# Kernel tuning notes

Measured on AMD Instinct MI355X. Metric: run time of the kernel, lower is better.

Reference implementation:

```python
import jax, jax.numpy as jnp
import numpy as np
from jax import lax

D_MODEL = 768
BATCH = 16
SEQ = 2048
N_BLOCKS = D_MODEL // 3
LN_EPS = 1e-5


def setup_inputs() -> dict:
    key = jax.random.key(0)
    ks = jax.random.split(key, 4)
    scale = 1.0 / np.sqrt(D_MODEL)
    x = jax.random.normal(ks[0], (BATCH, SEQ, D_MODEL), dtype=jnp.float32)
    W_biv = jax.random.normal(ks[1], (D_MODEL, D_MODEL), dtype=jnp.float32) * scale
    b_biv = jnp.zeros((D_MODEL,), dtype=jnp.float32)
    W_decay = jax.random.normal(ks[2], (1, D_MODEL), dtype=jnp.float32) * scale
    b_decay = jnp.full((1,), 1.4, dtype=jnp.float32)  # nn.init.constant_(decay_proj.bias, 1.4)
    W_in = jax.random.normal(ks[3], (D_MODEL, D_MODEL), dtype=jnp.float32) * scale
    b_in = jnp.zeros((D_MODEL,), dtype=jnp.float32)
    ln_gamma = jnp.ones((D_MODEL,), dtype=jnp.float32)
    ln_beta = jnp.zeros((D_MODEL,), dtype=jnp.float32)
    return {"x": x, "W_biv": W_biv, "b_biv": b_biv, "W_decay": W_decay,
            "b_decay": b_decay, "W_in": W_in, "b_in": b_in,
            "ln_gamma": ln_gamma, "ln_beta": ln_beta}


def _quat_rotate_blocks(h_blocks, biv):
    """h_blocks, biv: (batch, n_blocks, 3) -> rotated (batch, n_blocks, 3)."""
    norm_b = jnp.maximum(jnp.linalg.norm(biv, axis=-1, keepdims=True), 1e-8)
    half = norm_b * 0.5
    w = jnp.cos(half)[..., 0]
    s = (jnp.sin(half) / norm_b)[..., 0]
    # note the original maps bivector components in reversed order
    qx = s * biv[..., 2]
    qy = -s * biv[..., 1]
    qz = s * biv[..., 0]
    vx, vy, vz = h_blocks[..., 0], h_blocks[..., 1], h_blocks[..., 2]
    tx = 2.0 * (qy * vz - qz * vy)
    ty = 2.0 * (qz * vx - qx * vz)
    tz = 2.0 * (qx * vy - qy * vx)
    rx = vx + w * tx + (qy * tz - qz * ty)
    ry = vy + w * ty + (qz * tx - qx * tz)
    rz = vz + w * tz + (qx * ty - qy * tx)
    return jnp.stack([rx, ry, rz], axis=-1)


def reference(x, W_biv, b_biv, W_decay, b_decay, W_in, b_in, ln_gamma, ln_beta):
    B, S, D = x.shape
    nb = D // 3
    # precompute all per-timestep projections as big GEMMs
    biv = (jnp.einsum('bsd,ed->bse', x, W_biv) + b_biv).reshape(B, S, nb, 3)
    decay = jax.nn.sigmoid(jnp.einsum('bsd,ed->bse', x, W_decay) + b_decay)  # (B,S,1)
    inj = jnp.einsum('bsd,ed->bse', x, W_in) + b_in  # (B,S,D)

    def step(h, t):
        biv_t, decay_t, inj_t = t
        rot = _quat_rotate_blocks(h.reshape(B, nb, 3), biv_t).reshape(B, D)
        h_next = decay_t * rot + inj_t
        return h_next, h_next

    xs = (jnp.moveaxis(biv, 1, 0), jnp.moveaxis(decay, 1, 0), jnp.moveaxis(inj, 1, 0))
    h0 = jnp.zeros((B, D), dtype=x.dtype)
    _, out = lax.scan(step, h0, xs)  # (S,B,D)
    out = jnp.moveaxis(out, 0, 1)  # (B,S,D)

    mean = jnp.mean(out, axis=-1, keepdims=True)
    var = jnp.mean(jnp.square(out - mean), axis=-1, keepdims=True)
    normed = (out - mean) * lax.rsqrt(var + LN_EPS) * ln_gamma + ln_beta
    return normed + x
```

## Files before the change

kernel.cpp:

```cpp
#include <hip/hip_runtime.h>
#include <stdint.h>

#define D_MODEL 768
#define BATCH   16
#define SEQ     2048
#define M_ROWS  (BATCH * SEQ)
#define LN_EPS  1e-5f

#define CHUNKS  64
#define CLEN    (SEQ / CHUNKS)
#define PFB     8

typedef __attribute__((ext_vector_type(4))) float        f32x4;
typedef __attribute__((ext_vector_type(8))) __bf16       bf16x8;
typedef __attribute__((ext_vector_type(2))) unsigned int u32x2;

__device__ __forceinline__ unsigned short f2bf(float f) {
    union { float f; uint32_t u; } v; v.f = f;
    uint32_t u = v.u;
    uint32_t r = (u + 0x7FFFu + ((u >> 16) & 1u)) >> 16;
    return (unsigned short)r;
}
__device__ __forceinline__ float bf2f(unsigned short u) {
    union { uint32_t u; float f; } v; v.u = (uint32_t)u << 16; return v.f;
}
__device__ __forceinline__ float bfx(u32x2 v, int k) {
    unsigned int w = (k & 2) ? v[1] : v[0];
    return bf2f((unsigned short)(w >> ((k & 1) * 16)));
}

__device__ __forceinline__ void gload_lds16(const void* g, void* l) {
    __builtin_amdgcn_global_load_lds(
        (const __attribute__((address_space(1))) unsigned int*)g,
        (__attribute__((address_space(3))) unsigned int*)l,
        16, 0, 0);
}

__global__ __launch_bounds__(256) void k_conv_decay(
    const float* __restrict__ x, const float* __restrict__ Wd,
    const float* __restrict__ bd, unsigned short* __restrict__ xb,
    float* __restrict__ decay)
{
    int row = blockIdx.x;
    int i   = threadIdx.x;
    const float* xr = x + (size_t)row * D_MODEL;
    float v0 = xr[i], v1 = xr[i + 256], v2 = xr[i + 512];
    unsigned short* xbr = xb + (size_t)row * D_MODEL;
    xbr[i] = f2bf(v0); xbr[i + 256] = f2bf(v1); xbr[i + 512] = f2bf(v2);

    float part = v0 * Wd[i] + v1 * Wd[i + 256] + v2 * Wd[i + 512];
    #pragma unroll
    for (int off = 32; off; off >>= 1) part += __shfl_down(part, off);
    __shared__ float wsum[4];
    int wid = i >> 6, lane = i & 63;
    if (lane == 0) wsum[wid] = part;
    __syncthreads();
    if (i == 0) {
        float s = wsum[0] + wsum[1] + wsum[2] + wsum[3] + bd[0];
        decay[row] = 1.f / (1.f + __expf(-s));
    }
}

__global__ __launch_bounds__(256) void k_conv_w(
    const float* __restrict__ Wb, const float* __restrict__ Wi,
    unsigned short* __restrict__ Wdst)
{
    const int NW = D_MODEL * D_MODEL;
    int g = blockIdx.x * 256 + threadIdx.x;
    int base = g * 4;
    unsigned short* dst = Wdst + base;
    const float* src;
    if (base < NW) { src = Wb + base; }
    else           { src = Wi + (base - NW); }
    float4 v = *(const float4*)src;
    ushort4 o;
    o.x = f2bf(v.x); o.y = f2bf(v.y); o.z = f2bf(v.z); o.w = f2bf(v.w);
    *(ushort4*)dst = o;
}

#define GBM 256
#define GBN 256
#define GNBX 6
#define GNBY 128
#define NT   12

__global__ __launch_bounds__(512, 2) void k_gemm_fused(
    const unsigned short* __restrict__ A,
    const unsigned short* __restrict__ Bw,
    const float* __restrict__ bias_biv, const float* __restrict__ bias_in,
    u32x2* __restrict__ bivq, u32x2* __restrict__ injq)
{
    extern __shared__ unsigned short LDSBUF[];
    unsigned short* LA = LDSBUF;
    unsigned short* LB = LDSBUF + 32768;

    int id  = blockIdx.x;
    int swz = (id & 7) * 96 + (id >> 3);
    int bxc = swz % GNBX, byr = swz / GNBX;
    int m0 = byr * GBM, n0 = bxc * GBN;

    int tid  = threadIdx.x;
    int wid  = tid >> 6, lane = tid & 63;
    int wm = wid >> 2, wn = wid & 3;
    int rl = lane & 15, kq = lane >> 4;
    int sl = kq ^ ((rl >> 1) & 3);
    int aoff = (wm * 128 + rl) * 32 + sl * 8;
    int boff = (wn * 64  + rl) * 32 + sl * 8;

    f32x4 acc[8][4] = {};

    #define STAGE_HALF(DBUF, KT, HH) do {                                        \
        _Pragma("unroll")                                                        \
        for (int p = 0; p < 2; ++p) {                                            \
            int idx = p * 512 + tid;                                             \
            int row = idx >> 2;                                                  \
            int ss  = ((idx & 3) ^ ((idx >> 3) & 3)) * 8;  \
            gload_lds16(A  + (size_t)(m0 + row) * D_MODEL + (KT) * 64 + (HH) * 32 + ss, \
                        LA + (DBUF) * 16384 + (HH) * 8192 + idx * 8);            \
            gload_lds16(Bw + (size_t)(n0 + row) * D_MODEL + (KT) * 64 + (HH) * 32 + ss, \
                        LB + (DBUF) * 16384 + (HH) * 8192 + idx * 8);            \
        }                                                                        \
    } while (0)

    #define PHASE(D, H, DOSTAGE, SBUF, SKT, SHH, WAITSTR) do {                   \
        bf16x8 af[8], bfv[4];                                                    \
        const unsigned short* pa = LA + (D) * 16384 + (H) * 8192 + aoff;         \
        const unsigned short* pb = LB + (D) * 16384 + (H) * 8192 + boff;         \
        _Pragma("unroll")                                                        \
        for (int i = 0; i < 8; ++i) af[i]  = *(const bf16x8*)(pa + i * 512);     \
        _Pragma("unroll")                                                        \
        for (int j = 0; j < 4; ++j) bfv[j] = *(const bf16x8*)(pb + j * 512);     \
        if (DOSTAGE) STAGE_HALF(SBUF, SKT, SHH);                                 \
        asm volatile(WAITSTR ::: "memory");                                      \
        asm volatile("s_barrier" ::: "memory");                                  \
        asm volatile("s_waitcnt lgkmcnt(0)" ::: "memory");                       \
        __builtin_amdgcn_sched_barrier(0);                                       \
        __builtin_amdgcn_s_setprio(1);                                           \
        _Pragma("unroll")                                                        \
        for (int i = 0; i < 8; ++i)                                              \
            _Pragma("unroll")                                                    \
            for (int j = 0; j < 4; ++j)                                          \
                acc[i][j] = __builtin_amdgcn_mfma_f32_16x16x32_bf16(             \
                    af[i], bfv[j], acc[i][j], 0, 0, 0);                          \
        __builtin_amdgcn_s_setprio(0);                                           \
        asm volatile("s_barrier" ::: "memory");                                  \
    } while (0)

    STAGE_HALF(0, 0, 0);
    STAGE_HALF(0, 0, 1);
    STAGE_HALF(1, 1, 0);
    asm volatile("s_waitcnt vmcnt(8)" ::: "memory");
    asm volatile("s_barrier" ::: "memory");

    for (int t = 0; t < 10; ++t) {
        int cur = t & 1;
        PHASE(cur, 0, true, cur ^ 1, t + 1, 1, "s_waitcnt vmcnt(8)");
        PHASE(cur, 1, true, cur,     t + 2, 0, "s_waitcnt vmcnt(8)");
    }
    PHASE(0, 0, true,  1, 11, 1, "s_waitcnt vmcnt(8)");
    PHASE(0, 1, false, 0, 0,  0, "s_waitcnt vmcnt(4)");
    PHASE(1, 0, false, 0, 0,  0, "s_waitcnt vmcnt(0)");
    PHASE(1, 1, false, 0, 0,  0, "");

    #undef PHASE
    #undef STAGE_HALF

    u32x2* Cq; const float* bias; int nloc;
    if (n0 < D_MODEL) { Cq = bivq; bias = bias_biv; nloc = n0; }
    else              { Cq = injq; bias = bias_in;  nloc = n0 - D_MODEL; }
    int cl = lane & 15;
    int qbase = (m0 >> 2) + wm * 32 + (lane >> 4);
    #pragma unroll
    for (int j = 0; j < 4; ++j) {
        int col = nloc + wn * 64 + j * 16 + cl;
        float bs = bias[col];
        #pragma unroll
        for (int i = 0; i < 8; ++i) {
            f32x4 a = acc[i][j];
            unsigned int lo = (unsigned int)f2bf(a[0] + bs) | ((unsigned int)f2bf(a[1] + bs) << 16);
            unsigned int hi = (unsigned int)f2bf(a[2] + bs) | ((unsigned int)f2bf(a[3] + bs) << 16);
            u32x2 pk = {lo, hi};
            Cq[(size_t)(qbase + i * 4) * D_MODEL + col] = pk;
        }
    }
}

#define QSTEP_CORE(BX,BY,BZ, IX,IY,IZ, DD)                              \
    {   float n2   = (BX)*(BX) + (BY)*(BY) + (BZ)*(BZ);                 \
        float nrm  = fmaxf(__builtin_sqrtf(n2), 1e-8f);                 \
        float half = 0.5f * nrm;                                        \
        float w = __cosf(half);                                         \
        float s = __sinf(half) / nrm;                                   \
        float qx = s * (BZ), qy = -s * (BY), qz = s * (BX);             \
        float tx = 2.f * (qy * hz - qz * hy);                           \
        float ty = 2.f * (qz * hx - qx * hz);                           \
        float tz = 2.f * (qx * hy - qy * hx);                           \
        float rx = hx + w * tx + (qy * tz - qz * ty);                   \
        float ry = hy + w * ty + (qz * tx - qx * tz);                   \
        float rz = hz + w * tz + (qx * ty - qy * tx);                   \
        hx = fmaf((DD), rx, (IX));                                      \
        hy = fmaf((DD), ry, (IY));                                      \
        hz = fmaf((DD), rz, (IZ));                                      \
        float nQw = w * Qw - qx * Qx - qy * Qy - qz * Qz;               \
        float nQx = w * Qx + Qw * qx + (qy * Qz - qz * Qy);             \
        float nQy = w * Qy + Qw * qy + (qz * Qx - qx * Qz);             \
        float nQz = w * Qz + Qw * qz + (qx * Qy - qy * Qx);             \
        Qw = nQw; Qx = nQx; Qy = nQy; Qz = nQz;                         \
        S *= (DD);                                                      \
    }

#define QSTEP_H(BX,BY,BZ, IX,IY,IZ, DD)                                 \
    {   float n2   = (BX)*(BX) + (BY)*(BY) + (BZ)*(BZ);                 \
        float nrm  = fmaxf(__builtin_sqrtf(n2), 1e-8f);                 \
        float half = 0.5f * nrm;                                        \
        float w = __cosf(half);                                         \
        float s = __sinf(half) / nrm;                                   \
        float qx = s * (BZ), qy = -s * (BY), qz = s * (BX);             \
        float tx = 2.f * (qy * hz - qz * hy);                           \
        float ty = 2.f * (qz * hx - qx * hz);                           \
        float tz = 2.f * (qx * hy - qy * hx);                           \
        float rx = hx + w * tx + (qy * tz - qz * ty);                   \
        float ry = hy + w * ty + (qz * tx - qx * tz);                   \
        float rz = hz + w * tz + (qx * ty - qy * tx);                   \
        hx = fmaf((DD), rx, (IX));                                      \
        hy = fmaf((DD), ry, (IY));                                      \
        hz = fmaf((DD), rz, (IZ));                                      \
    }

__global__ __launch_bounds__(256) void k_scan_p1(
    const u32x2* __restrict__ bivq, const u32x2* __restrict__ injq,
    const float* __restrict__ decay,
    float* __restrict__ ops)
{
    int j = threadIdx.x;
    int c = blockIdx.x & (CHUNKS - 1);
    int b = blockIdx.x >> 6;
    size_t qrow = ((size_t)b * SEQ + (size_t)c * CLEN) >> 2;
    const u32x2* bv = bivq + qrow * D_MODEL + 3 * j;
    const u32x2* ij = injq + qrow * D_MODEL + 3 * j;
    const float* dk = decay + (size_t)b * SEQ + c * CLEN;

    u32x2 Ab0, Ab1, Ab2, Ai0, Ai1, Ai2; f32x4 Ad;
    u32x2 Bb0, Bb1, Bb2, Bi0, Bi1, Bi2; f32x4 Bd;

    #define LOADQ1(P, q)                                                  \
        P##b0 = bv[(size_t)(q) * D_MODEL + 0];                            \
        P##b1 = bv[(size_t)(q) * D_MODEL + 1];                            \
        P##b2 = bv[(size_t)(q) * D_MODEL + 2];                            \
        P##i0 = ij[(size_t)(q) * D_MODEL + 0];                            \
        P##i1 = ij[(size_t)(q) * D_MODEL + 1];                            \
        P##i2 = ij[(size_t)(q) * D_MODEL + 2];                            \
        P##d  = *(const f32x4*)(dk + (q) * 4);

    #define PROC41(P)                                                     \
        _Pragma("unroll")                                                 \
        for (int k = 0; k < 4; ++k) {                                     \
            float bx = bfx(P##b0, k), by = bfx(P##b1, k), bz = bfx(P##b2, k); \
            float ix = bfx(P##i0, k), iy = bfx(P##i1, k), iz = bfx(P##i2, k); \
            float d = P##d[k];                                            \
            QSTEP_CORE(bx, by, bz, ix, iy, iz, d)                         \
        }

    float hx = 0.f, hy = 0.f, hz = 0.f;
    float Qw = 1.f, Qx = 0.f, Qy = 0.f, Qz = 0.f, S = 1.f;

    LOADQ1(A, 0)
    LOADQ1(B, 1)
    #pragma unroll
    for (int q0 = 0; q0 < CLEN / 4; q0 += 2) {
        PROC41(A)
        if (q0 + 2 < CLEN / 4) { LOADQ1(A, q0 + 2) }
        PROC41(B)
        if (q0 + 3 < CLEN / 4) { LOADQ1(B, q0 + 3) }
    }
    #undef LOADQ1
    #undef PROC41

    float* op = ops + ((size_t)(b * CHUNKS + c) * 256 + j) * 8;
    f32x4 o0 = {Qw, Qx, Qy, Qz};
    f32x4 o1 = {S, hx, hy, hz};
    *(f32x4*)op = o0;
    *(f32x4*)(op + 4) = o1;
}

__global__ __launch_bounds__(64) void k_scan_p2(
    const float* __restrict__ ops, float* __restrict__ hs)
{
    int gid = blockIdx.x * 64 + threadIdx.x;
    int j = gid & 255, b = gid >> 8;

    float q0[PFB], q1[PFB], q2[PFB], q3[PFB], sc[PFB], o0[PFB], o1[PFB], o2[PFB];
    #pragma unroll
    for (int p = 0; p < PFB; ++p) {
        const float* op = ops + ((size_t)(b * CHUNKS + p) * 256 + j) * 8;
        f32x4 a = *(const f32x4*)op, bb = *(const f32x4*)(op + 4);
        q0[p] = a[0]; q1[p] = a[1]; q2[p] = a[2]; q3[p] = a[3];
        sc[p] = bb[0]; o0[p] = bb[1]; o1[p] = bb[2]; o2[p] = bb[3];
    }
    float hx = 0.f, hy = 0.f, hz = 0.f;
    for (int c0 = 0; c0 < CHUNKS; c0 += PFB) {
        #pragma unroll
        for (int p = 0; p < PFB; ++p) {
            int c = c0 + p;
            float* h = hs + ((size_t)(b * CHUNKS + c) * 256 + j) * 3;
            h[0] = hx; h[1] = hy; h[2] = hz;
            float w = q0[p], qx = q1[p], qy = q2[p], qz = q3[p];
            float s = sc[p], bx = o0[p], by = o1[p], bz = o2[p];
            int cn = c + PFB;
            if (cn < CHUNKS) {
                const float* op = ops + ((size_t)(b * CHUNKS + cn) * 256 + j) * 8;
                f32x4 a = *(const f32x4*)op, bb = *(const f32x4*)(op + 4);
                q0[p] = a[0]; q1[p] = a[1]; q2[p] = a[2]; q3[p] = a[3];
                sc[p] = bb[0]; o0[p] = bb[1]; o1[p] = bb[2]; o2[p] = bb[3];
            }
            float tx = 2.f * (qy * hz - qz * hy);
            float ty = 2.f * (qz * hx - qx * hz);
            float tz = 2.f * (qx * hy - qy * hx);
            float rx = hx + w * tx + (qy * tz - qz * ty);
            float ry = hy + w * ty + (qz * tx - qx * tz);
            float rz = hz + w * tz + (qx * ty - qy * tx);
            hx = fmaf(s, rx, bx);
            hy = fmaf(s, ry, by);
            hz = fmaf(s, rz, bz);
        }
    }
}

__global__ __launch_bounds__(256) void k_scan_p3(
    const u32x2* __restrict__ bivq, const u32x2* __restrict__ injq,
    const float* __restrict__ decay, const float* __restrict__ hs,
    const float* __restrict__ x, const float* __restrict__ gamma,
    const float* __restrict__ beta, float* __restrict__ out)
{
    int blk = blockIdx.x;
    int c = blk & (CHUNKS - 1);
    int b = blk >> 6;
    int j = threadIdx.x;
    size_t row0 = (size_t)b * SEQ + (size_t)c * CLEN;
    size_t qrow = row0 >> 2;
    const u32x2* bv = bivq + qrow * D_MODEL + 3 * j;
    const u32x2* ij = injq + qrow * D_MODEL + 3 * j;
    const float* dk = decay + row0;
    const float* h0 = hs + ((size_t)(b * CHUNKS + c) * 256 + j) * 3;
    float hx = h0[0], hy = h0[1], hz = h0[2];

    __shared__ uint32_t       hxyS[CLEN * 256];
    __shared__ unsigned short hzS [CLEN * 256];

    u32x2 Ab0, Ab1, Ab2, Ai0, Ai1, Ai2; f32x4 Ad;
    u32x2 Bb0, Bb1, Bb2, Bi0, Bi1, Bi2; f32x4 Bd;

    #define LOADQH(P, q)                                                  \
        P##b0 = bv[(size_t)(q) * D_MODEL + 0];                            \
        P##b1 = bv[(size_t)(q) * D_MODEL + 1];                            \
        P##b2 = bv[(size_t)(q) * D_MODEL + 2];                            \
        P##i0 = ij[(size_t)(q) * D_MODEL + 0];                            \
        P##i1 = ij[(size_t)(q) * D_MODEL + 1];                            \
        P##i2 = ij[(size_t)(q) * D_MODEL + 2];                            \
        P##d  = *(const f32x4*)(dk + (q) * 4);

    #define PROC4H(P, QBASE)                                              \
        _Pragma("unroll")                                                 \
        for (int k = 0; k < 4; ++k) {                                     \
            float bx = bfx(P##b0, k), by = bfx(P##b1, k), bz = bfx(P##b2, k); \
            float ix = bfx(P##i0, k), iy = bfx(P##i1, k), iz = bfx(P##i2, k); \
            float d = P##d[k];                                            \
            QSTEP_H(bx, by, bz, ix, iy, iz, d)                            \
            int tt = (QBASE) * 4 + k;                                     \
            hxyS[tt * 256 + j] = (uint32_t)f2bf(hx) | ((uint32_t)f2bf(hy) << 16); \
            hzS [tt * 256 + j] = f2bf(hz);                                \
        }

    LOADQH(A, 0)
    LOADQH(B, 1)
    #pragma unroll
    for (int q0 = 0; q0 < CLEN / 4; q0 += 2) {
        PROC4H(A, q0)
        if (q0 + 2 < CLEN / 4) { LOADQH(A, q0 + 2) }
        PROC4H(B, q0 + 1)
        if (q0 + 3 < CLEN / 4) { LOADQH(B, q0 + 3) }
    }
    #undef LOADQH
    #undef PROC4H

    __syncthreads();

    int wid = j >> 6, lane = j & 63;
    const float4* g4 = (const float4*)(gamma + lane * 12);
    const float4* e4 = (const float4*)(beta  + lane * 12);
    float4 G0 = g4[0], G1 = g4[1], G2 = g4[2];
    float4 E0 = e4[0], E1 = e4[1], E2 = e4[2];
    const float* xbase = x   + row0 * D_MODEL;
    float*       obase = out + row0 * D_MODEL;

    for (int r = wid; r < CLEN; r += 4) {
        uint4   hv = *(const uint4*)  &hxyS[r * 256 + 4 * lane];
        ushort4 zv = *(const ushort4*)&hzS [r * 256 + 4 * lane];
        float h[12];
        h[0]  = bf2f((unsigned short)(hv.x & 0xFFFF)); h[1]  = bf2f((unsigned short)(hv.x >> 16)); h[2]  = bf2f(zv.x);
        h[3]  = bf2f((unsigned short)(hv.y & 0xFFFF)); h[4]  = bf2f((unsigned short)(hv.y >> 16)); h[5]  = bf2f(zv.y);
        h[6]  = bf2f((unsigned short)(hv.z & 0xFFFF)); h[7]  = bf2f((unsigned short)(hv.z >> 16)); h[8]  = bf2f(zv.z);
        h[9]  = bf2f((unsigned short)(hv.w & 0xFFFF)); h[10] = bf2f((unsigned short)(hv.w >> 16)); h[11] = bf2f(zv.w);
        float sp = 0.f, qp = 0.f;
        #pragma unroll
        for (int k = 0; k < 12; ++k) { sp += h[k]; qp += h[k] * h[k]; }
        #pragma unroll
        for (int off = 1; off < 64; off <<= 1) {
            sp += __shfl_xor(sp, off);
            qp += __shfl_xor(qp, off);
        }
        float mean = sp * (1.f / 768.f);
        float var  = qp * (1.f / 768.f) - mean * mean;
        float rstd = rsqrtf(var + LN_EPS);

        const float* xr2 = xbase + (size_t)r * D_MODEL + lane * 12;
        float*       or2 = obase + (size_t)r * D_MODEL + lane * 12;
        float4 X0 = *(const float4*)(xr2 + 0);
        float4 X1 = *(const float4*)(xr2 + 4);
        float4 X2 = *(const float4*)(xr2 + 8);
        float4 O0, O1, O2;
        O0.x = (h[0]  - mean) * rstd * G0.x + E0.x + X0.x;
        O0.y = (h[1]  - mean) * rstd * G0.y + E0.y + X0.y;
        O0.z = (h[2]  - mean) * rstd * G0.z + E0.z + X0.z;
        O0.w = (h[3]  - mean) * rstd * G0.w + E0.w + X0.w;
        O1.x = (h[4]  - mean) * rstd * G1.x + E1.x + X1.x;
        O1.y = (h[5]  - mean) * rstd * G1.y + E1.y + X1.y;
        O1.z = (h[6]  - mean) * rstd * G1.z + E1.z + X1.z;
        O1.w = (h[7]  - mean) * rstd * G1.w + E1.w + X1.w;
        O2.x = (h[8]  - mean) * rstd * G2.x + E2.x + X2.x;
        O2.y = (h[9]  - mean) * rstd * G2.y + E2.y + X2.y;
        O2.z = (h[10] - mean) * rstd * G2.z + E2.z + X2.z;
        O2.w = (h[11] - mean) * rstd * G2.w + E2.w + X2.w;
        *(float4*)(or2 + 0) = O0;
        *(float4*)(or2 + 4) = O1;
        *(float4*)(or2 + 8) = O2;
    }
}

extern "C" void kernel_launch(void* const* d_in, const int* in_sizes, int n_in,
                              void* d_out, int out_size, void* d_ws, size_t ws_size,
                              hipStream_t stream) {
    const float* x     = (const float*)d_in[0];
    const float* W_biv = (const float*)d_in[1];
    const float* b_biv = (const float*)d_in[2];
    const float* W_dec = (const float*)d_in[3];
    const float* b_dec = (const float*)d_in[4];
    const float* W_in  = (const float*)d_in[5];
    const float* b_in  = (const float*)d_in[6];
    const float* gamma = (const float*)d_in[7];
    const float* beta  = (const float*)d_in[8];
    float* out = (float*)d_out;

    char* ws = (char*)d_ws;
    unsigned short* xb    = (unsigned short*)(ws);
    unsigned short* Wcat  = (unsigned short*)(ws + 50331648);
    float*          decay = (float*)         (ws + 52690944);
    u32x2*          bivq  = (u32x2*)         (ws + 52822016);
    u32x2*          injq  = (u32x2*)         (ws + 103153664);
    float*          ops   = (float*)(ws);
    float*          hs    = (float*)(ws + 8388608);

    (void)in_sizes; (void)n_in; (void)out_size; (void)ws_size;

    hipFuncSetAttribute((const void*)k_gemm_fused,
                        hipFuncAttributeMaxDynamicSharedMemorySize, 131072);

    k_conv_decay<<<M_ROWS, 256, 0, stream>>>(x, W_dec, b_dec, xb, decay);
    k_conv_w    <<<1152,   256, 0, stream>>>(W_biv, W_in, Wcat);
    k_gemm_fused<<<GNBX * GNBY, 512, 131072, stream>>>(xb, Wcat, b_biv, b_in, bivq, injq);
    k_scan_p1   <<<1024, 256, 0, stream>>>(bivq, injq, decay, ops);
    k_scan_p2   <<<64,   64,  0, stream>>>(ops, hs);
    k_scan_p3   <<<1024, 256, 0, stream>>>(bivq, injq, decay, hs, x, gamma, beta, out);
}
```

Baseline: 221.3 us.

## Split GEMM K-loop into finer subphases and read bf16 residual in scan

The GEMM main loop now runs in quarter-size subphases: each computes half the M tile, loads the B fragments once per half-K and issues a single staging unit per subphase. This is meant to cut register pressure and interleave global-to-LDS loads more finely with MFMA work. Separately, the final scan kernel reads the residual x from the bf16 copy instead of fp32, and the chunk carry states are stored as bf16 with ops placed in the output buffer. Both halve residual and state traffic but add bf16 rounding error to the residual and the carried hidden state.

Result: faster. 210.7 us (-4.8%).

```diff
diff --git a/kernel.cpp b/kernel.cpp
--- a/kernel.cpp
+++ b/kernel.cpp
@@ -82,7 +82,6 @@
 #define GBN 256
 #define GNBX 6
 #define GNBY 128
-#define NT   12
 
 __global__ __launch_bounds__(512, 2) void k_gemm_fused(
     const unsigned short* __restrict__ A,
@@ -108,62 +107,69 @@
     int boff = (wn * 64  + rl) * 32 + sl * 8;
 
     f32x4 acc[8][4] = {};
-
-    #define STAGE_HALF(DBUF, KT, HH) do {                                        \
+    bf16x8 bfv[4];
+
+    #define STAGE_UNIT(DBUF, KT, H, RH) do {                                     \
+        int idx = (RH) * 512 + tid;                                              \
+        int row = idx >> 2;                                                      \
+        int ss  = ((idx & 3) ^ ((idx >> 3) & 3)) * 8;      \
+        gload_lds16(A  + (size_t)(m0 + row) * D_MODEL + (KT) * 64 + (H) * 32 + ss, \
+                    LA + (DBUF) * 16384 + (H) * 8192 + idx * 8);                 \
+        gload_lds16(Bw + (size_t)(n0 + row) * D_MODEL + (KT) * 64 + (H) * 32 + ss, \
+                    LB + (DBUF) * 16384 + (H) * 8192 + idx * 8);                 \
+    } while (0)
+
+    #define SUBPHASE(D, H, MH, DOSTAGE, SKT, SH, SRH, WAITSTR) do {              \
+        const unsigned short* pa = LA + (D) * 16384 + (H) * 8192 + aoff + (MH) * 2048; \
+        const unsigned short* pb = LB + (D) * 16384 + (H) * 8192 + boff;         \
+        bf16x8 af[4];                                                            \
         _Pragma("unroll")                                                        \
-        for (int p = 0; p < 2; ++p) {                                            \
-            int idx = p * 512 + tid;                                             \
-            int row = idx >> 2;                                                  \
-            int ss  = ((idx & 3) ^ ((idx >> 3) & 3)) * 8;  \
-            gload_lds16(A  + (size_t)(m0 + row) * D_MODEL + (KT) * 64 + (HH) * 32 + ss, \
-                        LA + (DBUF) * 16384 + (HH) * 8192 + idx * 8);            \
-            gload_lds16(Bw + (size_t)(n0 + row) * D_MODEL + (KT) * 64 + (HH) * 32 + ss, \
-                        LB + (DBUF) * 16384 + (HH) * 8192 + idx * 8);            \
+        for (int i = 0; i < 4; ++i) af[i] = *(const bf16x8*)(pa + i * 512);      \
+        if ((MH) == 0) {                                                         \
+            _Pragma("unroll")                                                    \
+            for (int j = 0; j < 4; ++j) bfv[j] = *(const bf16x8*)(pb + j * 512); \
         }                                                                        \
-    } while (0)
-
-    #define PHASE(D, H, DOSTAGE, SBUF, SKT, SHH, WAITSTR) do {                   \
-        bf16x8 af[8], bfv[4];                                                    \
-        const unsigned short* pa = LA + (D) * 16384 + (H) * 8192 + aoff;         \
-        const unsigned short* pb = LB + (D) * 16384 + (H) * 8192 + boff;         \
-        _Pragma("unroll")                                                        \
-        for (int i = 0; i < 8; ++i) af[i]  = *(const bf16x8*)(pa + i * 512);     \
-        _Pragma("unroll")                                                        \
-        for (int j = 0; j < 4; ++j) bfv[j] = *(const bf16x8*)(pb + j * 512);     \
-        if (DOSTAGE) STAGE_HALF(SBUF, SKT, SHH);                                 \
+        if (DOSTAGE) STAGE_UNIT((D) ^ 1, SKT, SH, SRH);                          \
         asm volatile(WAITSTR ::: "memory");                                      \
         asm volatile("s_barrier" ::: "memory");                                  \
         asm volatile("s_waitcnt lgkmcnt(0)" ::: "memory");                       \
         __builtin_amdgcn_sched_barrier(0);                                       \
         __builtin_amdgcn_s_setprio(1);                                           \
         _Pragma("unroll")                                                        \
-        for (int i = 0; i < 8; ++i)                                              \
+        for (int i = 0; i < 4; ++i)                                              \
             _Pragma("unroll")                                                    \
             for (int j = 0; j < 4; ++j)                                          \
-                acc[i][j] = __builtin_amdgcn_mfma_f32_16x16x32_bf16(             \
-                    af[i], bfv[j], acc[i][j], 0, 0, 0);                          \
+                acc[(MH) * 4 + i][j] = __builtin_amdgcn_mfma_f32_16x16x32_bf16(  \
+                    af[i], bfv[j], acc[(MH) * 4 + i][j], 0, 0, 0);               \
         __builtin_amdgcn_s_setprio(0);                                           \
         asm volatile("s_barrier" ::: "memory");                                  \
     } while (0)
 
-    STAGE_HALF(0, 0, 0);
-    STAGE_HALF(0, 0, 1);
-    STAGE_HALF(1, 1, 0);
-    asm volatile("s_waitcnt vmcnt(8)" ::: "memory");
+    STAGE_UNIT(0, 0, 0, 0);
+    STAGE_UNIT(0, 0, 0, 1);
+    STAGE_UNIT(0, 0, 1, 0);
+    STAGE_UNIT(0, 0, 1, 1);
+    asm volatile("s_waitcnt vmcnt(4)" ::: "memory");
     asm volatile("s_barrier" ::: "memory");
 
-    for (int t = 0; t < 10; ++t) {
-        int cur = t & 1;
-        PHASE(cur, 0, true, cur ^ 1, t + 1, 1, "s_waitcnt vmcnt(8)");
-        PHASE(cur, 1, true, cur,     t + 2, 0, "s_waitcnt vmcnt(8)");
-    }
-    PHASE(0, 0, true,  1, 11, 1, "s_waitcnt vmcnt(8)");
-    PHASE(0, 1, false, 0, 0,  0, "s_waitcnt vmcnt(4)");
-    PHASE(1, 0, false, 0, 0,  0, "s_waitcnt vmcnt(0)");
-    PHASE(1, 1, false, 0, 0,  0, "");
-
-    #undef PHASE
-    #undef STAGE_HALF
+    for (int kt = 0; kt < 10; ++kt) {
+        int D = kt & 1;
+        SUBPHASE(D, 0, 0, true, kt + 1, 0, 0, "");
+        SUBPHASE(D, 0, 1, true, kt + 1, 0, 1, "s_waitcnt vmcnt(4)");
+        SUBPHASE(D, 1, 0, true, kt + 1, 1, 0, "");
+        SUBPHASE(D, 1, 1, true, kt + 1, 1, 1, "s_waitcnt vmcnt(4)");
+    }
+    SUBPHASE(0, 0, 0, true, 11, 0, 0, "");
+    SUBPHASE(0, 0, 1, true, 11, 0, 1, "s_waitcnt vmcnt(4)");
+    SUBPHASE(0, 1, 0, true, 11, 1, 0, "");
+    SUBPHASE(0, 1, 1, true, 11, 1, 1, "s_waitcnt vmcnt(4)");
+    SUBPHASE(1, 0, 0, false, 0, 0, 0, "");
+    SUBPHASE(1, 0, 1, false, 0, 0, 0, "s_waitcnt vmcnt(0)");
+    SUBPHASE(1, 1, 0, false, 0, 0, 0, "");
+    SUBPHASE(1, 1, 1, false, 0, 0, 0, "");
+
+    #undef SUBPHASE
+    #undef STAGE_UNIT
 
     u32x2* Cq; const float* bias; int nloc;
     if (n0 < D_MODEL) { Cq = bivq; bias = bias_biv; nloc = n0; }
@@ -284,7 +290,7 @@
 }
 
 __global__ __launch_bounds__(64) void k_scan_p2(
-    const float* __restrict__ ops, float* __restrict__ hs)
+    const float* __restrict__ ops, unsigned short* __restrict__ hsb)
 {
     int gid = blockIdx.x * 64 + threadIdx.x;
     int j = gid & 255, b = gid >> 8;
@@ -302,8 +308,8 @@
         #pragma unroll
         for (int p = 0; p < PFB; ++p) {
             int c = c0 + p;
-            float* h = hs + ((size_t)(b * CHUNKS + c) * 256 + j) * 3;
-            h[0] = hx; h[1] = hy; h[2] = hz;
+            unsigned short* h = hsb + ((size_t)(b * CHUNKS + c) * 256 + j) * 3;
+            h[0] = f2bf(hx); h[1] = f2bf(hy); h[2] = f2bf(hz);
             float w = q0[p], qx = q1[p], qy = q2[p], qz = q3[p];
             float s = sc[p], bx = o0[p], by = o1[p], bz = o2[p];
             int cn = c + PFB;
@@ -328,8 +334,8 @@
 
 __global__ __launch_bounds__(256) void k_scan_p3(
     const u32x2* __restrict__ bivq, const u32x2* __restrict__ injq,
-    const float* __restrict__ decay, const float* __restrict__ hs,
-    const float* __restrict__ x, const float* __restrict__ gamma,
+    const float* __restrict__ decay, const unsigned short* __restrict__ hsb,
+    const unsigned short* __restrict__ xb, const float* __restrict__ gamma,
     const float* __restrict__ beta, float* __restrict__ out)
 {
     int blk = blockIdx.x;
@@ -341,8 +347,8 @@
     const u32x2* bv = bivq + qrow * D_MODEL + 3 * j;
     const u32x2* ij = injq + qrow * D_MODEL + 3 * j;
     const float* dk = decay + row0;
-    const float* h0 = hs + ((size_t)(b * CHUNKS + c) * 256 + j) * 3;
-    float hx = h0[0], hy = h0[1], hz = h0[2];
+    const unsigned short* h0p = hsb + ((size_t)(b * CHUNKS + c) * 256 + j) * 3;
+    float hx = bf2f(h0p[0]), hy = bf2f(h0p[1]), hz = bf2f(h0p[2]);
 
     __shared__ uint32_t       hxyS[CLEN * 256];
     __shared__ unsigned short hzS [CLEN * 256];
@@ -390,8 +396,8 @@
     const float4* e4 = (const float4*)(beta  + lane * 12);
     float4 G0 = g4[0], G1 = g4[1], G2 = g4[2];
     float4 E0 = e4[0], E1 = e4[1], E2 = e4[2];
-    const float* xbase = x   + row0 * D_MODEL;
-    float*       obase = out + row0 * D_MODEL;
+    const unsigned short* xbase = xb  + row0 * D_MODEL;
+    float*                obase = out + row0 * D_MODEL;
 
     for (int r = wid; r < CLEN; r += 4) {
         uint4   hv = *(const uint4*)  &hxyS[r * 256 + 4 * lane];
@@ -413,24 +419,24 @@
         float var  = qp * (1.f / 768.f) - mean * mean;
         float rstd = rsqrtf(var + LN_EPS);
 
-        const float* xr2 = xbase + (size_t)r * D_MODEL + lane * 12;
-        float*       or2 = obase + (size_t)r * D_MODEL + lane * 12;
-        float4 X0 = *(const float4*)(xr2 + 0);
-        float4 X1 = *(const float4*)(xr2 + 4);
-        float4 X2 = *(const float4*)(xr2 + 8);
+        const unsigned short* xr2 = xbase + (size_t)r * D_MODEL + lane * 12;
+        float*                or2 = obase + (size_t)r * D_MODEL + lane * 12;
+        ushort4 Xa = *(const ushort4*)(xr2 + 0);
+        ushort4 Xb = *(const ushort4*)(xr2 + 4);
+        ushort4 Xc = *(const ushort4*)(xr2 + 8);
         float4 O0, O1, O2;
-        O0.x = (h[0]  - mean) * rstd * G0.x + E0.x + X0.x;
-        O0.y = (h[1]  - mean) * rstd * G0.y + E0.y + X0.y;
-        O0.z = (h[2]  - mean) * rstd * G0.z + E0.z + X0.z;
-        O0.w = (h[3]  - mean) * rstd * G0.w + E0.w + X0.w;
-        O1.x = (h[4]  - mean) * rstd * G1.x + E1.x + X1.x;
-        O1.y = (h[5]  - mean) * rstd * G1.y + E1.y + X1.y;
-        O1.z = (h[6]  - mean) * rstd * G1.z + E1.z + X1.z;
-        O1.w = (h[7]  - mean) * rstd * G1.w + E1.w + X1.w;
-        O2.x = (h[8]  - mean) * rstd * G2.x + E2.x + X2.x;
-        O2.y = (h[9]  - mean) * rstd * G2.y + E2.y + X2.y;
-        O2.z = (h[10] - mean) * rstd * G2.z + E2.z + X2.z;
-        O2.w = (h[11] - mean) * rstd * G2.w + E2.w + X2.w;
+        O0.x = (h[0]  - mean) * rstd * G0.x + E0.x + bf2f(Xa.x);
+        O0.y = (h[1]  - mean) * rstd * G0.y + E0.y + bf2f(Xa.y);
+        O0.z = (h[2]  - mean) * rstd * G0.z + E0.z + bf2f(Xa.z);
+        O0.w = (h[3]  - mean) * rstd * G0.w + E0.w + bf2f(Xa.w);
+        O1.x = (h[4]  - mean) * rstd * G1.x + E1.x + bf2f(Xb.x);
+        O1.y = (h[5]  - mean) * rstd * G1.y + E1.y + bf2f(Xb.y);
+        O1.z = (h[6]  - mean) * rstd * G1.z + E1.z + bf2f(Xb.z);
+        O1.w = (h[7]  - mean) * rstd * G1.w + E1.w + bf2f(Xb.w);
+        O2.x = (h[8]  - mean) * rstd * G2.x + E2.x + bf2f(Xc.x);
+        O2.y = (h[9]  - mean) * rstd * G2.y + E2.y + bf2f(Xc.y);
+        O2.z = (h[10] - mean) * rstd * G2.z + E2.z + bf2f(Xc.z);
+        O2.w = (h[11] - mean) * rstd * G2.w + E2.w + bf2f(Xc.w);
         *(float4*)(or2 + 0) = O0;
         *(float4*)(or2 + 4) = O1;
         *(float4*)(or2 + 8) = O2;
@@ -457,8 +463,8 @@
     float*          decay = (float*)         (ws + 52690944);
     u32x2*          bivq  = (u32x2*)         (ws + 52822016);
     u32x2*          injq  = (u32x2*)         (ws + 103153664);
-    float*          ops   = (float*)(ws);
-    float*          hs    = (float*)(ws + 8388608);
+    float*          ops   = (float*)d_out;
+    unsigned short* hsb   = (unsigned short*)(ws + 50331648);
 
     (void)in_sizes; (void)n_in; (void)out_size; (void)ws_size;
 
@@ -469,6 +475,6 @@
     k_conv_w    <<<1152,   256, 0, stream>>>(W_biv, W_in, Wcat);
     k_gemm_fused<<<GNBX * GNBY, 512, 131072, stream>>>(xb, Wcat, b_biv, b_in, bivq, injq);
     k_scan_p1   <<<1024, 256, 0, stream>>>(bivq, injq, decay, ops);
-    k_scan_p2   <<<64,   64,  0, stream>>>(ops, hs);
-    k_scan_p3   <<<1024, 256, 0, stream>>>(bivq, injq, decay, hs, x, gamma, beta, out);
-}
+    k_scan_p2   <<<64,   64,  0, stream>>>(ops, hsb);
+    k_scan_p3   <<<1024, 256, 0, stream>>>(bivq, injq, decay, hsb, xb, gamma, beta, out);
+}
```
